# Kernel tuning notes

Measured on AMD Instinct MI355X. Metric: run time of the kernel, lower is better.

The kernel has to match this reference:

```python
import jax, jax.numpy as jnp
import numpy as np
import math

SR, N_FFT, N_MELS = 16000, 512, 64
ATTACK_T, RELEASE_T, DELTA_T = 0.005, 0.05, 0.016
KNEE_W = 10.0
LIM_THRESH = 90.0
THRESH_VAL, RATIO_VAL, LLG_VAL = 45.0, 3.0, 10.0
EPS = 1e-8


def _hz_to_mel(f):
    return 2595.0 * np.log10(1.0 + f / 700.0)


def _mel_to_hz(m):
    return 700.0 * (10.0 ** (m / 2595.0) - 1.0)


def _mel_filterbank(sr, n_fft, n_mels):
    n_freq = n_fft // 2 + 1
    freqs = np.linspace(0.0, sr / 2.0, n_freq)
    mpts = np.linspace(_hz_to_mel(0.0), _hz_to_mel(sr / 2.0), n_mels + 2)
    hz = _mel_to_hz(mpts)
    fb = np.zeros((n_mels, n_freq), dtype=np.float32)
    for m in range(n_mels):  # loop over fixed small n_mels, not data dims
        lo, ctr, hi = hz[m], hz[m + 1], hz[m + 2]
        up = (freqs - lo) / max(ctr - lo, 1e-6)
        dn = (hi - freqs) / max(hi - ctr, 1e-6)
        fb[m] = np.maximum(0.0, np.minimum(up, dn))
    return fb


def setup_inputs() -> dict:
    key = jax.random.key(0)
    B, T, F = 16, 6000, N_FFT // 2 + 1
    # STFT magnitude spectrum (positive), scaled so dB levels span the knee regions
    x = jax.random.uniform(key, (B, T, F), dtype=jnp.float32, minval=1e-3, maxval=200.0)
    mel_fb = jnp.asarray(_mel_filterbank(SR, N_FFT, N_MELS))  # [M, F]
    return {"x": x, "mel_fb": mel_fb}


def _wdrc_forward(x, mel_fb):
    dtype = x.dtype
    th = jnp.full((N_MELS,), THRESH_VAL, dtype)
    ra = jnp.full((N_MELS,), RATIO_VAL, dtype)
    llg = jnp.full((N_MELS,), LLG_VAL, dtype)
    kw = KNEE_W

    # 1) mel-scale power in dB
    power = x * x                                        # [B,T,F]
    mel_p = jnp.einsum('btf,mf->btm', power, mel_fb)     # [B,T,M]
    xdb = 10.0 * jnp.log10(mel_p + EPS)

    # 2) AREMA temporal smoothing (attack/release EMA, data-dependent coeff)
    a_c = jnp.asarray(1.0 - math.exp(-DELTA_T / ATTACK_T), dtype)
    r_c = jnp.asarray(1.0 - math.exp(-DELTA_T / RELEASE_T), dtype)

    def step(y_prev, x_t):
        alpha = jnp.where(x_t - y_prev > 0, a_c, r_c)
        y = alpha * x_t + (1.0 - alpha) * y_prev
        return y, y

    x_tbm = jnp.moveaxis(xdb, 1, 0)                      # [T,B,M]
    _, y_tbm = jax.lax.scan(step, jnp.zeros_like(x_tbm[0]), x_tbm)
    xG = jnp.moveaxis(y_tbm, 0, 1)                       # [B,T,M] smoothed levels (dB)

    # 3) soft-knee compressor (gain in dB)
    x1 = th - kw / 2.0
    x2 = th + kw / 2.0
    y1 = x1 + llg
    y2 = th + (x2 - th) / ra
    slope = (y2 - y1) / (x2 - x1)
    low_m = (th - kw / 2.0 - xG > 0).astype(dtype)
    comp_m = (xG - th - kw / 2.0 > 0).astype(dtype)
    knee_m = 1.0 - (low_m + comp_m)
    yG = (xG + llg) * low_m + (th + (xG - th) / ra) * comp_m + (y1 + slope * (xG - x1)) * knee_m
    xGc = yG  # = compressor gain + xG

    # 4) limiter
    lt = LIM_THRESH
    lim_m = (2.0 * (xGc - lt) - kw > 0).astype(dtype)
    yL = lt * lim_m + xGc * (1.0 - lim_m)
    tr_m = (kw - 2.0 * jnp.abs(xGc - lt) > 0).astype(dtype)
    c1 = lt - kw / 2.0
    c2 = kw * 2.0
    yL = (xGc - (xGc - c1) ** 2 / c2) * tr_m + yL * (1.0 - tr_m)

    # 5) overall mel-domain gain -> linear -> STFT-domain gain -> apply
    gain_db = yL - xG                                    # [B,T,M]
    gain_lin = 10.0 ** (gain_db / 20.0)
    fb_norm = mel_fb / (jnp.sum(mel_fb, axis=0, keepdims=True) + EPS)  # [M,F]
    gain_f = jnp.einsum('btm,mf->btf', gain_lin, fb_norm)              # [B,T,F]
    return x * gain_f


def reference(x, mel_fb):
    return _wdrc_forward(x, mel_fb)
```

## Files before the change

### kernel.cpp

```cpp
#include <hip/hip_runtime.h>
#include <math.h>

#define B_ 16
#define T_ 6000
#define F_ 257
#define M_ 64
#define R_ (B_*T_)

#define CHUNKS 48
#define CLEN   (T_/CHUNKS)
#define WARM   96

#define MAXSUP 32
#define TILE_R 32
#define TILE_E (TILE_R*F_)

#define ACF 0.9592377960216338f
#define RCF 0.27385096292630914f

__global__ void wdrc_prep(const float* __restrict__ fb,
                          float4* __restrict__ t_tab,
                          int* __restrict__ t_fs,
                          float* __restrict__ t_wm) {
    int tid = threadIdx.x;
    for (int f = tid; f < F_; f += blockDim.x) {
        float s = 0.f; int c = 0; int i0 = 0, i1 = 0; float v0 = 0.f, v1 = 0.f;
        for (int m = 0; m < M_; ++m) {
            float v = fb[m*F_ + f];
            s += v;
            if (v > 0.f) {
                if (c == 0) { i0 = m; v0 = v; }
                else if (c == 1) { i1 = m; v1 = v; }
                ++c;
            }
        }
        float inv = 1.0f / (s + 1e-8f);
        float w0 = v0*inv, w1 = v1*inv;
        if (c == 0) { i0 = 0; i1 = 0; w0 = 0.f; w1 = 0.f; }
        else if (c == 1) { i1 = i0; w1 = 0.f; }
        t_tab[f] = make_float4(w0, w1, __int_as_float(i0), __int_as_float(i1));
    }
    if (tid < M_) {
        int m = tid, lo = -1, hi = -1;
        for (int f = 0; f < F_; ++f)
            if (fb[m*F_ + f] > 0.f) { if (lo < 0) lo = f; hi = f; }
        int fs  = (lo < 0) ? 0 : lo;
        int len = (lo < 0) ? 0 : (hi - lo + 1);
        if (len > MAXSUP) len = MAXSUP;
        t_fs[m] = fs;
        for (int i = 0; i < MAXSUP; ++i)
            t_wm[i*M_ + m] = (i < len) ? fb[m*F_ + fs + i] : 0.f;
    }
}

__global__ __launch_bounds__(256) void wdrc_mel(const float* __restrict__ x,
                                                float* __restrict__ xdb,
                                                const int* __restrict__ t_fs,
                                                const float* __restrict__ t_wm) {
    __shared__ float xs[TILE_E + MAXSUP];
    __shared__ float wms[MAXSUP*M_];
    __shared__ int   fss[M_];
    int tid = threadIdx.x;
    int r0  = blockIdx.x * TILE_R;

    const float4* src4 = (const float4*)(x + (size_t)r0 * F_);
    float4* dst4 = (float4*)xs;
    #pragma unroll
    for (int k = 0; k < 9; ++k) {
        int i = tid + k*256;
        if (i < TILE_E/4) dst4[i] = src4[i];
    }
    if (tid < MAXSUP) xs[TILE_E + tid] = 0.f;
    for (int i = tid; i < MAXSUP*M_; i += 256) wms[i] = t_wm[i];
    if (tid < M_) fss[tid] = t_fs[tid];
    __syncthreads();

    int w = tid >> 6, m = tid & 63;
    int fs = fss[m];
    #pragma unroll
    for (int rr = w; rr < TILE_R; rr += 4) {
        const float* row = &xs[rr*F_ + fs];
        float acc = 0.f;
        #pragma unroll
        for (int i = 0; i < MAXSUP; ++i) {
            float v = row[i];
            acc = fmaf(v*v, wms[i*M_ + m], acc);
        }
        xdb[(size_t)(r0 + rr)*M_ + m] = 3.0102999566398120f * log2f(acc + 1e-8f);
    }
}

__global__ __launch_bounds__(256) void wdrc_scan(const float* __restrict__ xdb,
                                                 float* __restrict__ gl) {
    int tid = threadIdx.x;
    int wid = blockIdx.x * 4 + (tid >> 6);
    int m   = tid & 63;
    int b   = wid / CHUNKS;
    int c   = wid - b*CHUNKS;
    int ts  = c * CLEN, te = ts + CLEN;
    int tw  = ts - WARM; if (tw < 0) tw = 0;
    const size_t rowb = (size_t)b * T_;

    const float ac1 = 1.0f - ACF, rc1 = 1.0f - RCF;
    const float y2v   = 45.0f + 5.0f/3.0f;
    const float slope = (y2v - 50.0f) * 0.1f;

    float y = 0.f;
    float cur[8], nxt[8];
    #pragma unroll
    for (int i = 0; i < 8; ++i) {
        int t = tw + i; if (t >= te) t = te - 1;
        cur[i] = xdb[(rowb + t)*M_ + m];
    }
    for (int tb = tw; tb < te; tb += 8) {
        #pragma unroll
        for (int i = 0; i < 8; ++i) {
            int t = tb + 8 + i; if (t >= te) t = te - 1;
            nxt[i] = xdb[(rowb + t)*M_ + m];
        }
        #pragma unroll
        for (int i = 0; i < 8; ++i) {
            int t = tb + i;
            if (t < te) {
                float xv = cur[i];
                float d  = xv - y;
                bool  up = d > 0.f;
                float a  = up ? ACF : RCF;
                float b1 = up ? ac1 : rc1;
                y = fmaf(a, xv, b1 * y);
                if (t >= ts) {
                    float xG = y;
                    float yG;
                    if      (xG < 40.0f) yG = xG + 10.0f;
                    else if (xG > 50.0f) yG = fmaf(xG - 45.0f, 0.3333333333333333f, 45.0f);
                    else                 yG = fmaf(xG - 40.0f, slope, 50.0f);
                    float xGc = yG;
                    float yL  = (xGc > 95.0f) ? 90.0f : xGc;
                    float ad  = fabsf(xGc - 90.0f);
                    if (ad < 5.0f) { float u = xGc - 85.0f; yL = xGc - u*u*0.05f; }
                    float gd = yL - xG;
                    gl[(rowb + t)*M_ + m] = exp2f(gd * 0.16609640474436813f);
                }
            }
        }
        #pragma unroll
        for (int i = 0; i < 8; ++i) cur[i] = nxt[i];
    }
}

#define NV4 (R_*F_/4)
__global__ __launch_bounds__(256) void wdrc_apply(const float* __restrict__ x,
                                                  const float* __restrict__ gl,
                                                  float* __restrict__ out,
                                                  const float4* __restrict__ t_tab) {
    __shared__ float4 stab[F_];
    int tid = threadIdx.x;
    for (int i = tid; i < F_; i += 256) stab[i] = t_tab[i];
    __syncthreads();

    const float4* x4 = (const float4*)x;
    float4* o4 = (float4*)out;
    int stride = gridDim.x * blockDim.x;
    for (int v = blockIdx.x*blockDim.x + tid; v < NV4; v += stride) {
        float4 xv = x4[v];
        float xi[4] = {xv.x, xv.y, xv.z, xv.w};
        float ov[4];
        int n0 = v*4;
        #pragma unroll
        for (int e = 0; e < 4; ++e) {
            int idx = n0 + e;
            int r = (int)((unsigned)idx / 257u);
            int f = idx - r*257;
            float4 tb = stab[f];
            const float* glr = gl + (size_t)r*M_;
            int m0 = __float_as_int(tb.z), m1 = __float_as_int(tb.w);
            float g = tb.x*glr[m0] + tb.y*glr[m1];
            ov[e] = xi[e] * g;
        }
        o4[v] = make_float4(ov[0], ov[1], ov[2], ov[3]);
    }
}

extern "C" void kernel_launch(void* const* d_in, const int* in_sizes, int n_in,
                              void* d_out, int out_size, void* d_ws, size_t ws_size,
                              hipStream_t stream) {
    const float* x  = (const float*)d_in[0];
    const float* fb = (const float*)d_in[1];
    float* out = (float*)d_out;

    float*  xdb   = (float*)d_ws;
    float*  gl    = xdb + (size_t)R_*M_;
    float4* t_tab = (float4*)(gl + (size_t)R_*M_);
    int*    t_fs  = (int*)(t_tab + F_);
    float*  t_wm  = (float*)(t_fs + M_);

    size_t needed = (size_t)R_*M_*2*4 + F_*16 + M_*4 + MAXSUP*M_*4;
    if (ws_size < needed) return;

    wdrc_prep<<<1, 256, 0, stream>>>(fb, t_tab, t_fs, t_wm);
    wdrc_mel<<<R_/TILE_R, 256, 0, stream>>>(x, xdb, t_fs, t_wm);
    wdrc_scan<<<(B_*CHUNKS)/4, 256, 0, stream>>>(xdb, gl);
    wdrc_apply<<<2048, 256, 0, stream>>>(x, gl, out, t_tab);
}
```

Before: 307.7 us.

## Tile apply kernel per 32 rows with LDS gain cache and precomputed quad tables

The apply kernel now processes 32-row tiles and stages their mel gains in shared memory. It uses per-float4 precomputed weight and offset tables, which removes the per-element integer division and scattered global gain loads. The mel kernel stores squared spectra in a padded 260-float row stride so it can read them as aligned float4s, and keeps the filter weights in registers. The prep kernel builds the extra tables, which adds complexity and a slow-path fallback for float4s that span rows.

```diff
diff --git a/kernel.cpp b/kernel.cpp
--- a/kernel.cpp
+++ b/kernel.cpp
@@ -11,82 +11,130 @@
 #define CLEN   (T_/CHUNKS)
 #define WARM   96
 
-#define MAXSUP 32
-#define TILE_R 32
-#define TILE_E (TILE_R*F_)
-
 #define ACF 0.9592377960216338f
 #define RCF 0.27385096292630914f
 
-__global__ void wdrc_prep(const float* __restrict__ fb,
-                          float4* __restrict__ t_tab,
-                          int* __restrict__ t_fs,
-                          float* __restrict__ t_wm) {
-    int tid = threadIdx.x;
-    for (int f = tid; f < F_; f += blockDim.x) {
+#define TILE_R 32
+#define LSTR   260
+#define WSUP   32
+
+__global__ __launch_bounds__(256) void wdrc_prep(const float* __restrict__ fb,
+    float4* __restrict__ t_tab, float4* __restrict__ cw0, float4* __restrict__ cw1,
+    float4* __restrict__ cmeta, int* __restrict__ t_fs, float* __restrict__ t_wm)
+{
+    __shared__ float4 tabs[F_];
+    __shared__ int    slo[4*M_];
+    __shared__ int    sfa[M_];
+    int tid = threadIdx.x;
+
+    for (int f = tid; f < F_; f += 256) {
         float s = 0.f; int c = 0; int i0 = 0, i1 = 0; float v0 = 0.f, v1 = 0.f;
         for (int m = 0; m < M_; ++m) {
             float v = fb[m*F_ + f];
             s += v;
-            if (v > 0.f) {
-                if (c == 0) { i0 = m; v0 = v; }
-                else if (c == 1) { i1 = m; v1 = v; }
-                ++c;
-            }
-        }
-        float inv = 1.0f / (s + 1e-8f);
+            if (v > 0.f) { if (c==0){i0=m;v0=v;} else if (c==1){i1=m;v1=v;} ++c; }
+        }
+        float inv = 1.0f/(s + 1e-8f);
         float w0 = v0*inv, w1 = v1*inv;
-        if (c == 0) { i0 = 0; i1 = 0; w0 = 0.f; w1 = 0.f; }
-        else if (c == 1) { i1 = i0; w1 = 0.f; }
-        t_tab[f] = make_float4(w0, w1, __int_as_float(i0), __int_as_float(i1));
+        if (c == 0) { i0 = (f >= 128) ? 63 : 0; i1 = i0 + 1; w0 = 0.f; w1 = 0.f; }
+        else if (c == 1) { i1 = i0 + 1; w1 = 0.f; }
+        float4 tv = make_float4(w0, w1, __int_as_float(i0), __int_as_float(i1));
+        tabs[f] = tv; t_tab[f] = tv;
+    }
+    {
+        int m = tid & 63, seg = tid >> 6;
+        int f0 = seg*65, f1 = f0 + 65; if (f1 > F_) f1 = F_;
+        int lo = 0x7fffffff;
+        for (int f = f0; f < f1; ++f)
+            if (fb[m*F_ + f] > 0.f) { lo = f; break; }
+        slo[seg*M_ + m] = lo;
+    }
+    __syncthreads();
+    for (int j = tid; j < F_; j += 256) {
+        int f0 = 4*j; f0 -= 257*(f0/257);
+        int fast = (f0 < 254);
+        float4 tv0 = tabs[f0];
+        int a = __float_as_int(tv0.z);
+        float w0e[4], w1e[4]; int offp = 0;
+        for (int e = 0; e < 4; ++e) {
+            int fe = f0 + e; if (fe > 256) fe = 256;
+            float4 t = tabs[fe];
+            int off = __float_as_int(t.z) - a;
+            if (off < 0) off = 0; if (off > 3) off = 3;
+            offp |= off << (8*e);
+            w0e[e] = t.x; w1e[e] = t.y;
+        }
+        cw0[j] = make_float4(w0e[0], w0e[1], w0e[2], w0e[3]);
+        cw1[j] = make_float4(w1e[0], w1e[1], w1e[2], w1e[3]);
+        cmeta[j] = make_float4(__int_as_float(a), __int_as_float(offp),
+                               __int_as_float(fast), 0.f);
     }
     if (tid < M_) {
-        int m = tid, lo = -1, hi = -1;
-        for (int f = 0; f < F_; ++f)
-            if (fb[m*F_ + f] > 0.f) { if (lo < 0) lo = f; hi = f; }
-        int fs  = (lo < 0) ? 0 : lo;
-        int len = (lo < 0) ? 0 : (hi - lo + 1);
-        if (len > MAXSUP) len = MAXSUP;
-        t_fs[m] = fs;
-        for (int i = 0; i < MAXSUP; ++i)
-            t_wm[i*M_ + m] = (i < len) ? fb[m*F_ + fs + i] : 0.f;
+        int lo = slo[tid];
+        for (int s2 = 1; s2 < 4; ++s2) { int v = slo[s2*M_ + tid]; if (v < lo) lo = v; }
+        if (lo == 0x7fffffff) lo = 0;
+        int fa = lo & ~3;
+        sfa[tid] = fa; t_fs[tid] = fa;
+    }
+    __syncthreads();
+    {
+        int m = tid & 63;
+        int fa = sfa[m];
+        for (int i = tid >> 6; i < WSUP; i += 4) {
+            int f = fa + i;
+            t_wm[i*M_ + m] = (f < F_) ? fb[m*F_ + f] : 0.f;
+        }
     }
 }
 
 __global__ __launch_bounds__(256) void wdrc_mel(const float* __restrict__ x,
-                                                float* __restrict__ xdb,
-                                                const int* __restrict__ t_fs,
-                                                const float* __restrict__ t_wm) {
-    __shared__ float xs[TILE_E + MAXSUP];
-    __shared__ float wms[MAXSUP*M_];
+    float* __restrict__ xdb, const int* __restrict__ t_fs, const float* __restrict__ t_wm)
+{
+    __shared__ __align__(16) float xs[TILE_R*LSTR + 64];
+    __shared__ float wms[WSUP*M_];
     __shared__ int   fss[M_];
     int tid = threadIdx.x;
-    int r0  = blockIdx.x * TILE_R;
-
-    const float4* src4 = (const float4*)(x + (size_t)r0 * F_);
-    float4* dst4 = (float4*)xs;
+    size_t r0 = (size_t)blockIdx.x * TILE_R;
+
+    for (int i = tid; i < WSUP*M_; i += 256) wms[i] = t_wm[i];
+    if (tid < M_) fss[tid] = t_fs[tid];
+    for (int i = tid; i < TILE_R*3 + 64; i += 256) {
+        if (i < TILE_R*3) { int r = i/3; int c = i - 3*r; xs[r*LSTR + F_ + c] = 0.f; }
+        else xs[TILE_R*LSTR + (i - TILE_R*3)] = 0.f;
+    }
+    const float4* src4 = (const float4*)(x + r0*F_);
+    for (int c = tid; c < TILE_R*F_/4; c += 256) {
+        float4 v = src4[c];
+        float vv[4] = {v.x*v.x, v.y*v.y, v.z*v.z, v.w*v.w};
+        int g = 4*c;
+        #pragma unroll
+        for (int e = 0; e < 4; ++e) {
+            int idx = g + e;
+            int r = (int)((unsigned)idx / 257u);
+            int f = idx - 257*r;
+            xs[r*LSTR + f] = vv[e];
+        }
+    }
+    __syncthreads();
+
+    int m = tid & 63, w = tid >> 6;
+    int fa = fss[m];
+    float wr[WSUP];
     #pragma unroll
-    for (int k = 0; k < 9; ++k) {
-        int i = tid + k*256;
-        if (i < TILE_E/4) dst4[i] = src4[i];
-    }
-    if (tid < MAXSUP) xs[TILE_E + tid] = 0.f;
-    for (int i = tid; i < MAXSUP*M_; i += 256) wms[i] = t_wm[i];
-    if (tid < M_) fss[tid] = t_fs[tid];
-    __syncthreads();
-
-    int w = tid >> 6, m = tid & 63;
-    int fs = fss[m];
-    #pragma unroll
+    for (int i = 0; i < WSUP; ++i) wr[i] = wms[i*M_ + m];
+
     for (int rr = w; rr < TILE_R; rr += 4) {
-        const float* row = &xs[rr*F_ + fs];
+        const float4* px = (const float4*)&xs[rr*LSTR + fa];
         float acc = 0.f;
         #pragma unroll
-        for (int i = 0; i < MAXSUP; ++i) {
-            float v = row[i];
-            acc = fmaf(v*v, wms[i*M_ + m], acc);
-        }
-        xdb[(size_t)(r0 + rr)*M_ + m] = 3.0102999566398120f * log2f(acc + 1e-8f);
+        for (int j = 0; j < 8; ++j) {
+            float4 q = px[j];
+            acc = fmaf(q.x, wr[4*j+0], acc);
+            acc = fmaf(q.y, wr[4*j+1], acc);
+            acc = fmaf(q.z, wr[4*j+2], acc);
+            acc = fmaf(q.w, wr[4*j+3], acc);
+        }
+        xdb[(r0 + rr)*M_ + m] = 3.0102999566398120f * log2f(acc + 1e-8f);
     }
 }
 
@@ -148,36 +196,67 @@
     }
 }
 
-#define NV4 (R_*F_/4)
 __global__ __launch_bounds__(256) void wdrc_apply(const float* __restrict__ x,
-                                                  const float* __restrict__ gl,
-                                                  float* __restrict__ out,
-                                                  const float4* __restrict__ t_tab) {
-    __shared__ float4 stab[F_];
-    int tid = threadIdx.x;
-    for (int i = tid; i < F_; i += 256) stab[i] = t_tab[i];
-    __syncthreads();
-
-    const float4* x4 = (const float4*)x;
-    float4* o4 = (float4*)out;
-    int stride = gridDim.x * blockDim.x;
-    for (int v = blockIdx.x*blockDim.x + tid; v < NV4; v += stride) {
-        float4 xv = x4[v];
-        float xi[4] = {xv.x, xv.y, xv.z, xv.w};
+    const float* __restrict__ gl, float* __restrict__ out,
+    const float4* __restrict__ t_tab, const float4* __restrict__ cw0,
+    const float4* __restrict__ cw1, const float4* __restrict__ cmeta)
+{
+    __shared__ __align__(16) float gls[32*68];
+    __shared__ float4 sw0[F_], sw1[F_], sme[F_], stab[F_];
+    int tid = threadIdx.x;
+    size_t r0 = (size_t)blockIdx.x * 32;
+
+    for (int i = tid; i < F_; i += 256) {
+        sw0[i] = cw0[i]; sw1[i] = cw1[i]; sme[i] = cmeta[i]; stab[i] = t_tab[i];
+    }
+    const float4* g4 = (const float4*)(gl + r0*M_);
+    for (int i = tid; i < 512; i += 256) {
+        float4 v = g4[i];
+        int r = i >> 4, c0 = (i & 15) << 2;
+        *(float4*)&gls[r*68 + c0] = v;
+    }
+    for (int i = tid; i < 128; i += 256) { int r = i >> 2; gls[r*68 + 64 + (i & 3)] = 0.f; }
+    __syncthreads();
+
+    const float4* x4 = (const float4*)(x + r0*F_);
+    float4*       o4 = (float4*)(out + r0*F_);
+    for (int i = tid; i < 2056; i += 256) {
+        float4 xv = x4[i];
+        int j = i - 257*(i/257);
+        int r = (int)((unsigned)(4*i) / 257u);
+        float4 me = sme[j];
+        float xe[4] = {xv.x, xv.y, xv.z, xv.w};
         float ov[4];
-        int n0 = v*4;
-        #pragma unroll
-        for (int e = 0; e < 4; ++e) {
-            int idx = n0 + e;
-            int r = (int)((unsigned)idx / 257u);
-            int f = idx - r*257;
-            float4 tb = stab[f];
-            const float* glr = gl + (size_t)r*M_;
-            int m0 = __float_as_int(tb.z), m1 = __float_as_int(tb.w);
-            float g = tb.x*glr[m0] + tb.y*glr[m1];
-            ov[e] = xi[e] * g;
-        }
-        o4[v] = make_float4(ov[0], ov[1], ov[2], ov[3]);
+        if (__float_as_int(me.z)) {
+            float4 w0 = sw0[j], w1 = sw1[j];
+            int a    = __float_as_int(me.x);
+            int offp = __float_as_int(me.y);
+            const float* gr = &gls[r*68 + a];
+            float g0 = gr[0], g1 = gr[1], g2 = gr[2], g3 = gr[3], gX = gr[4];
+            float w0a[4] = {w0.x, w0.y, w0.z, w0.w};
+            float w1a[4] = {w1.x, w1.y, w1.z, w1.w};
+            #pragma unroll
+            for (int e = 0; e < 4; ++e) {
+                int off = (offp >> (8*e)) & 3;
+                float ge  = off==0 ? g0 : off==1 ? g1 : off==2 ? g2 : g3;
+                float ge1 = off==0 ? g1 : off==1 ? g2 : off==2 ? g3 : gX;
+                float g = w0a[e]*ge + w1a[e]*ge1;
+                ov[e] = xe[e]*g;
+            }
+        } else {
+            int base = 4*i;
+            #pragma unroll
+            for (int e = 0; e < 4; ++e) {
+                int idx = base + e;
+                int rr = (int)((unsigned)idx / 257u);
+                int f  = idx - 257*rr;
+                float4 tb = stab[f];
+                int m0 = __float_as_int(tb.z), m1 = __float_as_int(tb.w);
+                float g = tb.x*gls[rr*68 + m0] + tb.y*gls[rr*68 + m1];
+                ov[e] = xe[e]*g;
+            }
+        }
+        o4[i] = make_float4(ov[0], ov[1], ov[2], ov[3]);
     }
 }
 
@@ -191,14 +270,17 @@
     float*  xdb   = (float*)d_ws;
     float*  gl    = xdb + (size_t)R_*M_;
     float4* t_tab = (float4*)(gl + (size_t)R_*M_);
-    int*    t_fs  = (int*)(t_tab + F_);
+    float4* cw0   = t_tab + F_;
+    float4* cw1   = cw0 + F_;
+    float4* cmeta = cw1 + F_;
+    int*    t_fs  = (int*)(cmeta + F_);
     float*  t_wm  = (float*)(t_fs + M_);
 
-    size_t needed = (size_t)R_*M_*2*4 + F_*16 + M_*4 + MAXSUP*M_*4;
+    size_t needed = (size_t)R_*M_*2*4 + (size_t)F_*16*4 + M_*4 + (size_t)WSUP*M_*4;
     if (ws_size < needed) return;
 
-    wdrc_prep<<<1, 256, 0, stream>>>(fb, t_tab, t_fs, t_wm);
+    wdrc_prep<<<1, 256, 0, stream>>>(fb, t_tab, cw0, cw1, cmeta, t_fs, t_wm);
     wdrc_mel<<<R_/TILE_R, 256, 0, stream>>>(x, xdb, t_fs, t_wm);
     wdrc_scan<<<(B_*CHUNKS)/4, 256, 0, stream>>>(xdb, gl);
-    wdrc_apply<<<2048, 256, 0, stream>>>(x, gl, out, t_tab);
-}
+    wdrc_apply<<<R_/32, 256, 0, stream>>>(x, gl, out, t_tab, cw0, cw1, cmeta);
+}
```

Result: faster. 294.8 us (-4.2%).
